# Kernel tuning notes

Measured on AMD Instinct MI355X. Metric: run time of the kernel, lower is better.

## Reference

```python
import jax, jax.numpy as jnp
import numpy as np

EPS = 1e-5  # BatchNorm1d default eps


def _proj_bn(x, W, gamma, beta, mean, var):
    # Conv1d(kernel=1, bias=False) == channel matmul, then inference BatchNorm1d.
    y = jnp.einsum('oc,bcn->bon', W, x)  # (B, C_out, N)
    scale = gamma / jnp.sqrt(var + EPS)  # (C_out,)
    shift = beta - mean * scale
    return y * scale[:, None] + shift[:, None]


def setup_inputs() -> dict:
    key = jax.random.key(0)
    ks = jax.random.split(key, 8)
    B, C, N = 8, 512, 2048
    inp = {
        'input': jax.random.normal(ks[0], (B, C, N), dtype=jnp.float32),
        'Wq': jax.random.normal(ks[1], (C, C), dtype=jnp.float32) * (1.0 / np.sqrt(C)),
        'gq': jnp.ones((C,), jnp.float32),
        'bq': jnp.zeros((C,), jnp.float32),
        'mq': jax.random.normal(ks[2], (C,), dtype=jnp.float32) * 0.1,
        'vq': jax.random.uniform(ks[3], (C,), dtype=jnp.float32) + 0.5,
        'Wk': jax.random.normal(ks[4], (C, C), dtype=jnp.float32) * (1.0 / np.sqrt(C)),
        'gk': jnp.ones((C,), jnp.float32),
        'bk': jnp.zeros((C,), jnp.float32),
        'mk': jax.random.normal(ks[5], (C,), dtype=jnp.float32) * 0.1,
        'vk': jax.random.uniform(ks[6], (C,), dtype=jnp.float32) + 0.5,
        'Wv': jax.random.normal(ks[7], (C, C), dtype=jnp.float32) * (1.0 / np.sqrt(C)),
        'gv': jnp.ones((C,), jnp.float32),
        'bv': jnp.zeros((C,), jnp.float32),
        'mv': jax.random.normal(jax.random.fold_in(key, 100), (C,), dtype=jnp.float32) * 0.1,
        'vv': jax.random.uniform(jax.random.fold_in(key, 101), (C,), dtype=jnp.float32) + 0.5,
    }
    return inp


def reference(input, Wq, gq, bq, mq, vq, Wk, gk, bk, mk, vk, Wv, gv, bv, mv, vv):
    q = _proj_bn(input, Wq, gq, bq, mq, vq)  # (B, C, N)
    k = _proj_bn(input, Wk, gk, bk, mk, vk)
    v = _proj_bn(input, Wv, gv, bv, mv, vv)
    # w[b, i, j] = sum_c q[b, c, i] * k[b, c, j]
    w = jnp.einsum('bci,bcj->bij', q, k)
    a = jax.nn.softmax(w, axis=-1)  # softmax over key axis j (dim 3 in torch)
    # c[b, c, i] = sum_j a[b, i, j] * v[b, c, j]  (== (v * w.softmax(3)).sum(3))
    return jnp.einsum('bij,bcj->bci', a, v)
```

## Files before the change

kernel.cpp:

```cpp
#include <hip/hip_runtime.h>
#include <cstdint>
#include <cstddef>

#define EPSV 1e-5f
constexpr int B_ = 8;
constexpr int C_ = 512;
constexpr int N_ = 2048;

typedef _Float16 f16x8 __attribute__((ext_vector_type(8)));
typedef float    f32x4 __attribute__((ext_vector_type(4)));

__device__ __forceinline__ unsigned short f16b(float f) {
    _Float16 h = (_Float16)f;
    return __builtin_bit_cast(unsigned short, h);
}

__device__ __forceinline__ void gload_lds16(const void* g, void* l) {
    __builtin_amdgcn_global_load_lds(
        (const __attribute__((address_space(1))) void*)g,
        (__attribute__((address_space(3))) void*)l, 16, 0, 0);
}

__global__ __launch_bounds__(256) void split_x_kernel(
    const float* __restrict__ x, unsigned short* __restrict__ xh)
{
    __shared__ float T[64][65];
    const int b = blockIdx.z, c0 = blockIdx.y * 64, n0 = blockIdx.x * 64;
    const float* xb = x + ((size_t)b * C_ + c0) * N_ + n0;
    const int tid = threadIdx.x;
    const int lr = tid >> 4;
    const int lcn = (tid & 15) * 4;
#pragma unroll
    for (int it = 0; it < 4; ++it) {
        float4 v = *(const float4*)&xb[(size_t)(lr + 16 * it) * N_ + lcn];
        T[lr + 16 * it][lcn + 0] = v.x;
        T[lr + 16 * it][lcn + 1] = v.y;
        T[lr + 16 * it][lcn + 2] = v.z;
        T[lr + 16 * it][lcn + 3] = v.w;
    }
    __syncthreads();
    const int n = tid >> 2, cb = (tid & 3) * 16;
    alignas(16) unsigned short h[16];
#pragma unroll
    for (int i = 0; i < 16; ++i)
        h[i] = f16b(T[cb + i][n]);
    const size_t o = ((size_t)b * N_ + n0 + n) * C_ + c0 + cb;
    *(uint4*)&xh[o]     = *(uint4*)&h[0];
    *(uint4*)&xh[o + 8] = *(uint4*)&h[8];
}

__global__ __launch_bounds__(256) void split_w_kernel(
    const float* __restrict__ W, unsigned short* __restrict__ wh)
{
    const int i = (blockIdx.x * 256 + threadIdx.x) * 4;
    float4 v = *(const float4*)&W[i];
    alignas(8) unsigned short h[4];
    h[0] = f16b(v.x); h[1] = f16b(v.y); h[2] = f16b(v.z); h[3] = f16b(v.w);
    *(ushort4*)&wh[i] = *(ushort4*)&h[0];
}

__global__ __launch_bounds__(512) void param_concat_kernel(
    const float* gq, const float* bq, const float* mq, const float* vq,
    const float* gk, const float* bk, const float* mk, const float* vk,
    const float* gv, const float* bv, const float* mv, const float* vv,
    float* sg, float* sb, float* sm, float* sv)
{
    const int i = threadIdx.x;
    sg[i] = gq[i];  sg[512 + i] = gk[i];  sg[1024 + i] = gv[i];
    sb[i] = bq[i];  sb[512 + i] = bk[i];  sb[1024 + i] = bv[i];
    sm[i] = mq[i];  sm[512 + i] = mk[i];  sm[1024 + i] = mv[i];
    sv[i] = vq[i];  sv[512 + i] = vk[i];  sv[1024 + i] = vv[i];
}

constexpr int EPI_QK = 0, EPI_PROJT = 2;

template <int EPI>
__global__ __launch_bounds__(512, 4) void qk256(
    const unsigned short* __restrict__ Ah, const unsigned short* __restrict__ Bh,
    int K, int lda, int ldb,
    long strideA, long strideB, long strideC, long strideC2,
    void* __restrict__ C0, void* __restrict__ C1, float* __restrict__ ML,
    const float* __restrict__ g, const float* __restrict__ bt,
    const float* __restrict__ mu, const float* __restrict__ var)
{
    __shared__ char smem[49152];

    const int id = blockIdx.x;
    const int bz = id & 7;
    const int s  = id >> 3;
    const int bx = s & 15, by = s >> 4;
    const int n0 = bx * 128;
    const int m0 = by * 256;

    const unsigned short* Ahb = Ah + (size_t)bz * strideA;
    const unsigned short* Bhb = Bh + (size_t)bz * strideB;

    const int tid  = threadIdx.x;
    const int lane = tid & 63;
    const int wv   = tid >> 6;
    const int wr   = wv >> 1, wc = wv & 1;
    const int WRB  = wr * 64, WCB = wc * 64;
    const int l4 = lane >> 4, l15 = lane & 15;

#define STAGE(t)                                                              \
    {                                                                         \
        char* dst = smem + ((t) & 1) * 24576;                                 \
        _Pragma("unroll")                                                     \
        for (int u = 0; u < 2; ++u) {                                         \
            const int L = u * 512 + tid;                                      \
            const int row = L >> 2;                                           \
            const int ssl = ((L & 3) ^ ((row >> 1) & 3)) * 8;                 \
            gload_lds16(Ahb + (size_t)(m0 + row) * lda + (t) * 32 + ssl,      \
                        dst + L * 16);                                        \
        }                                                                     \
        {                                                                     \
            const int row = tid >> 2;                                         \
            const int ssl = ((tid & 3) ^ ((row >> 1) & 3)) * 8;               \
            gload_lds16(Bhb + (size_t)(n0 + row) * ldb + (t) * 32 + ssl,      \
                        dst + 16384 + tid * 16);                              \
        }                                                                     \
    }

    f32x4 acc[4][4] = {};
    const int NT = K / 32;

    STAGE(0);

    for (int t = 0; t < NT; ++t) {
        char* cur = smem + (t & 1) * 24576;
        __builtin_amdgcn_s_barrier();
        if (t + 1 < NT) {
            STAGE(t + 1);
            asm volatile("s_waitcnt vmcnt(3)" ::: "memory");
        } else {
            asm volatile("s_waitcnt vmcnt(0)" ::: "memory");
        }
        __builtin_amdgcn_s_barrier();

        f16x8 ah[4], bh[4];
#pragma unroll
        for (int m = 0; m < 4; ++m) {
            const int row = WRB + m * 16 + l15;
            ah[m] = *(const f16x8*)(cur + row * 64 +
                                    ((l4 ^ ((row >> 1) & 3)) * 16));
        }
#pragma unroll
        for (int n = 0; n < 4; ++n) {
            const int row = WCB + n * 16 + l15;
            bh[n] = *(const f16x8*)(cur + 16384 + row * 64 +
                                    ((l4 ^ ((row >> 1) & 3)) * 16));
        }
        __builtin_amdgcn_s_setprio(1);
#pragma unroll
        for (int m = 0; m < 4; ++m)
#pragma unroll
            for (int n = 0; n < 4; ++n)
                acc[m][n] = __builtin_amdgcn_mfma_f32_16x16x32_f16(
                    ah[m], bh[n], acc[m][n], 0, 0, 0);
        __builtin_amdgcn_s_setprio(0);
    }
#undef STAGE

    if constexpr (EPI == EPI_QK) {
        unsigned short* H = (unsigned short*)C0 + (size_t)bz * strideC;
        const int tcol = bx * 2 + wc;
        const size_t mbase = (((size_t)bz * 32 + tcol) * 2) * 2048;
#pragma unroll
        for (int m = 0; m < 4; ++m) {
#pragma unroll
            for (int r = 0; r < 4; ++r) {
                float mx = fmaxf(fmaxf(acc[m][0][r], acc[m][1][r]),
                                 fmaxf(acc[m][2][r], acc[m][3][r]));
#pragma unroll
                for (int off = 1; off < 16; off <<= 1)
                    mx = fmaxf(mx, __shfl_xor(mx, off));
                float pe[4];
                float s2 = 0.f;
#pragma unroll
                for (int n = 0; n < 4; ++n) {
                    pe[n] = __expf(acc[m][n][r] - mx);
                    s2 += pe[n];
                }
#pragma unroll
                for (int off = 1; off < 16; off <<= 1)
                    s2 += __shfl_xor(s2, off);
                const int rloc = WRB + m * 16 + l4 * 4 + r;
                if (l15 == 0) {
                    ML[mbase + m0 + rloc] = mx;
                    ML[mbase + 2048 + m0 + rloc] = s2;
                }
#pragma unroll
                for (int n = 0; n < 4; ++n)
                    H[(size_t)(m0 + rloc) * 2048 + n0 + WCB + n * 16 + l15] =
                        f16b(pe[n]);
            }
        }
    } else {
        if (m0 < 1024) {
            unsigned short* H = (unsigned short*)C0 + (size_t)bz * strideC;
#pragma unroll
            for (int m = 0; m < 4; ++m) {
                const int mg = m0 + WRB + m * 16 + l4 * 4;
                float sc[4], sh[4];
#pragma unroll
                for (int r = 0; r < 4; ++r) {
                    const int o = mg + r;
                    sc[r] = g[o] * rsqrtf(var[o] + EPSV);
                    sh[r] = bt[o] - mu[o] * sc[r];
                }
#pragma unroll
                for (int n = 0; n < 4; ++n) {
                    const int ng = n0 + WCB + n * 16 + l15;
                    alignas(8) unsigned short h4[4];
#pragma unroll
                    for (int r = 0; r < 4; ++r)
                        h4[r] = f16b(acc[m][n][r] * sc[r] + sh[r]);
                    *(ushort4*)&H[(size_t)ng * 1024 + mg] = *(ushort4*)&h4[0];
                }
            }
        } else {
            unsigned short* V = (unsigned short*)C1 + (size_t)bz * strideC2;
#pragma unroll
            for (int m = 0; m < 4; ++m) {
                const int mg = m0 + WRB + m * 16 + l4 * 4;
                float sc[4], sh[4];
#pragma unroll
                for (int r = 0; r < 4; ++r) {
                    const int o = mg + r;
                    sc[r] = g[o] * rsqrtf(var[o] + EPSV);
                    sh[r] = bt[o] - mu[o] * sc[r];
                }
                const int d0 = mg - 1024;
#pragma unroll
                for (int n = 0; n < 4; ++n) {
                    const int ng = n0 + WCB + n * 16 + l15;
#pragma unroll
                    for (int r = 0; r < 4; ++r)
                        V[(size_t)(d0 + r) * 2048 + ng] =
                            f16b(acc[m][n][r] * sc[r] + sh[r]);
                }
            }
        }
    }
}

__global__ __launch_bounds__(512, 2) void pv256(
    const unsigned short* __restrict__ Ah, const unsigned short* __restrict__ Bh,
    int K, int lda, int ldb, long strideA, long strideB, long strideC,
    void* __restrict__ C0,
    const float* __restrict__ corr, const float* __restrict__ linv)
{
    constexpr int BUFSZ = 49152;
    __shared__ char smem[163840];

    const int id = blockIdx.x;
    const int bz = id & 7;
    const int s  = id >> 3;
    const int bx = s & 3, by = s >> 2;
    const int n0 = bx * 128;
    const int m0 = by * 256;

    const unsigned short* Ahb = Ah + (size_t)bz * strideA;
    const unsigned short* Bhb = Bh + (size_t)bz * strideB;

    const int tid  = threadIdx.x;
    const int lane = tid & 63;
    const int wv   = tid >> 6;
    const int wr   = wv >> 2, wc = wv & 3;
    const int WRB  = wr * 128, WCB = wc * 32;
    const int l4 = lane >> 4, l15 = lane & 15;

    const int srow = tid >> 3;
    const int sslot = ((tid & 7) ^ (srow & 7)) * 8;

    unsigned short* corrLds = (unsigned short*)(smem + 147456);
    for (int idx = tid; idx < 2048; idx += 512) {
        const int t = idx >> 6, i4 = (idx & 63) * 4;
        float4 c4 = *(const float4*)&corr[((size_t)bz * 32 + t) * 2048 + m0 + i4];
        alignas(8) unsigned short h4[4] =
            {f16b(c4.x), f16b(c4.y), f16b(c4.z), f16b(c4.w)};
        *(ushort4*)&corrLds[(size_t)t * 256 + i4] = *(ushort4*)&h4[0];
    }
    __syncthreads();

#define STAGE(t)                                                              \
    {                                                                         \
        char* dst = smem + ((t) % 3) * BUFSZ;                                 \
        const unsigned short* asrc =                                          \
            Ahb + (size_t)(m0 + srow) * lda + (t) * 64 + sslot;               \
        _Pragma("unroll")                                                     \
        for (int u = 0; u < 4; ++u)                                           \
            gload_lds16(asrc + (size_t)(u * 64) * lda,                        \
                        dst + u * 8192 + tid * 16);                           \
        const unsigned short* bsrc =                                          \
            Bhb + (size_t)(n0 + srow) * ldb + (t) * 64 + sslot;               \
        _Pragma("unroll")                                                     \
        for (int u = 0; u < 2; ++u)                                           \
            gload_lds16(bsrc + (size_t)(u * 64) * ldb,                        \
                        dst + 32768 + u * 8192 + tid * 16);                   \
    }

    f32x4 acc[8][2] = {};
    const int NT = K / 64;

    STAGE(0);
    STAGE(1);

    for (int t = 0; t < NT; ++t) {
        char* cur = smem + (t % 3) * BUFSZ;
        if (t + 2 < NT) {
            asm volatile("s_waitcnt vmcnt(6)" ::: "memory");
        } else {
            asm volatile("s_waitcnt vmcnt(0)" ::: "memory");
        }
        __builtin_amdgcn_s_barrier();
        asm volatile("" ::: "memory");
        if (t + 2 < NT) STAGE(t + 2);

        f16x8 ah[8][2], bh[2][2];
#pragma unroll
        for (int m = 0; m < 8; ++m) {
            const int row = WRB + m * 16 + l15;
#pragma unroll
            for (int kk = 0; kk < 2; ++kk)
                ah[m][kk] = *(const f16x8*)(cur + row * 128 +
                                            (((kk << 2) | l4) ^ (row & 7)) * 16);
        }
#pragma unroll
        for (int n = 0; n < 2; ++n) {
            const int row = WCB + n * 16 + l15;
#pragma unroll
            for (int kk = 0; kk < 2; ++kk)
                bh[n][kk] = *(const f16x8*)(cur + 32768 + row * 128 +
                                            (((kk << 2) | l4) ^ (row & 7)) * 16);
        }
#pragma unroll
        for (int m = 0; m < 8; ++m) {
            const _Float16 cf = ((const _Float16*)corrLds)
                [(size_t)t * 256 + WRB + m * 16 + l15];
            ah[m][0] = ah[m][0] * cf;
            ah[m][1] = ah[m][1] * cf;
        }
        __builtin_amdgcn_s_setprio(1);
#pragma unroll
        for (int kk = 0; kk < 2; ++kk)
#pragma unroll
            for (int m = 0; m < 8; ++m)
#pragma unroll
                for (int n = 0; n < 2; ++n)
                    acc[m][n] = __builtin_amdgcn_mfma_f32_16x16x32_f16(
                        ah[m][kk], bh[n][kk], acc[m][n], 0, 0, 0);
        __builtin_amdgcn_s_setprio(0);
    }
#undef STAGE

    float* Cb = (float*)C0 + (size_t)bz * strideC;
    const float* lb = linv + (size_t)bz * 2048;
#pragma unroll
    for (int m = 0; m < 8; ++m) {
        const int mrow = m0 + WRB + m * 16 + l4 * 4;
        float lv[4];
#pragma unroll
        for (int r = 0; r < 4; ++r)
            lv[r] = lb[mrow + r];
#pragma unroll
        for (int n = 0; n < 2; ++n) {
            const int col = n0 + WCB + n * 16 + l15;
            float4 o4 = make_float4(acc[m][n][0] * lv[0],
                                    acc[m][n][1] * lv[1],
                                    acc[m][n][2] * lv[2],
                                    acc[m][n][3] * lv[3]);
            *(float4*)&Cb[(size_t)col * 2048 + mrow] = o4;
        }
    }
}

__global__ __launch_bounds__(256) void ml_combine_kernel(
    const float* __restrict__ ml, float* __restrict__ corr,
    float* __restrict__ linv)
{
    const int idx = blockIdx.x * 256 + threadIdx.x;
    const int b = idx >> 11, i = idx & 2047;
    const float* base = ml + ((size_t)b * 32) * 2 * 2048 + i;
    float M = -3.0e38f;
#pragma unroll 8
    for (int t = 0; t < 32; ++t)
        M = fmaxf(M, base[(size_t)t * 4096]);
    float L = 0.f;
    float* cb = corr + (size_t)b * 32 * 2048 + i;
#pragma unroll 8
    for (int t = 0; t < 32; ++t) {
        const float c = __expf(base[(size_t)t * 4096] - M);
        L += c * base[(size_t)t * 4096 + 2048];
        cb[(size_t)t * 2048] = c;
    }
    linv[idx] = 1.0f / L;
}

extern "C" void kernel_launch(void* const* d_in, const int* in_sizes, int n_in,
                              void* d_out, int out_size, void* d_ws, size_t ws_size,
                              hipStream_t stream)
{
    (void)in_sizes; (void)n_in; (void)out_size; (void)ws_size;
    const float* x  = (const float*)d_in[0];
    const float* Wq = (const float*)d_in[1];
    const float* gq = (const float*)d_in[2];
    const float* bq = (const float*)d_in[3];
    const float* mq = (const float*)d_in[4];
    const float* vq = (const float*)d_in[5];
    const float* Wk = (const float*)d_in[6];
    const float* gk = (const float*)d_in[7];
    const float* bk = (const float*)d_in[8];
    const float* mk = (const float*)d_in[9];
    const float* vk = (const float*)d_in[10];
    const float* Wv = (const float*)d_in[11];
    const float* gv = (const float*)d_in[12];
    const float* bv = (const float*)d_in[13];
    const float* mv = (const float*)d_in[14];
    const float* vv = (const float*)d_in[15];
    float* out = (float*)d_out;

    const size_t MiB = 1048576;
    char* ws = (char*)d_ws;
    unsigned short* Wst = (unsigned short*)(ws);
    unsigned short* Wqh = Wst;
    unsigned short* Wkh = Wst + 512 * 512;
    unsigned short* Wvh = Wst + 1024 * 512;
    unsigned short* vbf  = (unsigned short*)(ws + 2 * MiB);
    unsigned short* qkTh = (unsigned short*)(ws + 18 * MiB);
    unsigned short* xTh  = (unsigned short*)(ws + 50 * MiB);
    unsigned short* pbuf = (unsigned short*)(ws + 66 * MiB);
    float* mlbuf = (float*)(ws + 130 * MiB);
    float* corr  = (float*)(ws + 134 * MiB);
    float* linv  = (float*)(ws + 136 * MiB);
    float* sg = (float*)(ws + 136 * MiB + 65536);
    float* sb = sg + 1536;
    float* sm = sb + 1536;
    float* sv = sm + 1536;

    const long BS = (long)N_ * C_;
    const long QKS = (long)N_ * 1024;

    split_x_kernel<<<dim3(N_ / 64, C_ / 64, B_), 256, 0, stream>>>(x, xTh);
    split_w_kernel<<<dim3(256), 256, 0, stream>>>(Wq, Wqh);
    split_w_kernel<<<dim3(256), 256, 0, stream>>>(Wk, Wkh);
    split_w_kernel<<<dim3(256), 256, 0, stream>>>(Wv, Wvh);
    param_concat_kernel<<<dim3(1), 512, 0, stream>>>(
        gq, bq, mq, vq, gk, bk, mk, vk, gv, bv, mv, vv, sg, sb, sm, sv);

    qk256<EPI_PROJT><<<dim3(768), 512, 0, stream>>>(
        Wst, xTh, 512, 512, 512, 0, BS, QKS, BS, qkTh, vbf,
        nullptr, sg, sb, sm, sv);

    qk256<EPI_QK><<<dim3(1024), 512, 0, stream>>>(
        qkTh, qkTh + 512, 512, 1024, 1024, QKS, QKS, (long)N_ * N_, 0,
        pbuf, nullptr, mlbuf, nullptr, nullptr, nullptr, nullptr);

    ml_combine_kernel<<<dim3(B_ * N_ / 256), 256, 0, stream>>>(
        mlbuf, corr, linv);

    pv256<<<dim3(256), 512, 0, stream>>>(
        pbuf, vbf, 2048, 2048, 2048, (long)N_ * N_, BS, BS, out, corr, linv);
}
```

Before: 169.4 us.

## Shrink PV tile to 128x128 with double buffering and fuse weight prep kernels

Replaces the 256x128, 512-thread, triple-buffered PV GEMM with a 128x128, 256-thread, double-buffered version launched on 512 blocks. Each wave now holds a 4x4 accumulator tile. The smaller shared-memory footprint should allow more blocks per CU and fill the GPU with more blocks. The three weight-conversion launches and the parameter concat launch are merged into one kernel to cut launch overhead. In exchange, each block reuses loaded data less, and prefetch depth drops from two stages ahead to one.

```diff
diff --git a/kernel.cpp b/kernel.cpp
--- a/kernel.cpp
+++ b/kernel.cpp
@@ -49,27 +49,34 @@
     *(uint4*)&xh[o + 8] = *(uint4*)&h[8];
 }
 
-__global__ __launch_bounds__(256) void split_w_kernel(
-    const float* __restrict__ W, unsigned short* __restrict__ wh)
-{
-    const int i = (blockIdx.x * 256 + threadIdx.x) * 4;
-    float4 v = *(const float4*)&W[i];
-    alignas(8) unsigned short h[4];
-    h[0] = f16b(v.x); h[1] = f16b(v.y); h[2] = f16b(v.z); h[3] = f16b(v.w);
-    *(ushort4*)&wh[i] = *(ushort4*)&h[0];
-}
-
-__global__ __launch_bounds__(512) void param_concat_kernel(
+__global__ __launch_bounds__(256) void split_w_all_kernel(
+    const float* __restrict__ Wq, const float* __restrict__ Wk,
+    const float* __restrict__ Wv, unsigned short* __restrict__ wst,
     const float* gq, const float* bq, const float* mq, const float* vq,
     const float* gk, const float* bk, const float* mk, const float* vk,
     const float* gv, const float* bv, const float* mv, const float* vv,
     float* sg, float* sb, float* sm, float* sv)
 {
-    const int i = threadIdx.x;
-    sg[i] = gq[i];  sg[512 + i] = gk[i];  sg[1024 + i] = gv[i];
-    sb[i] = bq[i];  sb[512 + i] = bk[i];  sb[1024 + i] = bv[i];
-    sm[i] = mq[i];  sm[512 + i] = mk[i];  sm[1024 + i] = mv[i];
-    sv[i] = vq[i];  sv[512 + i] = vk[i];  sv[1024 + i] = vv[i];
+    const int blk = blockIdx.x;
+    if (blk < 768) {
+        const int i = blk * 1024 + threadIdx.x * 4;
+        const int which = i >> 18;
+        const int off = i & 262143;
+        const float* W = (which == 0) ? Wq : (which == 1) ? Wk : Wv;
+        float4 v = *(const float4*)&W[off];
+        alignas(8) unsigned short h[4];
+        h[0] = f16b(v.x); h[1] = f16b(v.y); h[2] = f16b(v.z); h[3] = f16b(v.w);
+        *(ushort4*)&wst[i] = *(ushort4*)&h[0];
+    } else {
+#pragma unroll
+        for (int u = 0; u < 2; ++u) {
+            const int i = threadIdx.x + u * 256;
+            sg[i] = gq[i];  sg[512 + i] = gk[i];  sg[1024 + i] = gv[i];
+            sb[i] = bq[i];  sb[512 + i] = bk[i];  sb[1024 + i] = bv[i];
+            sm[i] = mq[i];  sm[512 + i] = mk[i];  sm[1024 + i] = mv[i];
+            sv[i] = vq[i];  sv[512 + i] = vk[i];  sv[1024 + i] = vv[i];
+        }
+    }
 }
 
 constexpr int EPI_QK = 0, EPI_PROJT = 2;
@@ -244,21 +251,20 @@
     }
 }
 
-__global__ __launch_bounds__(512, 2) void pv256(
+__global__ __launch_bounds__(256, 2) void pv128(
     const unsigned short* __restrict__ Ah, const unsigned short* __restrict__ Bh,
     int K, int lda, int ldb, long strideA, long strideB, long strideC,
     void* __restrict__ C0,
     const float* __restrict__ corr, const float* __restrict__ linv)
 {
-    constexpr int BUFSZ = 49152;
-    __shared__ char smem[163840];
+    __shared__ char smem[73728];
 
     const int id = blockIdx.x;
     const int bz = id & 7;
     const int s  = id >> 3;
     const int bx = s & 3, by = s >> 2;
     const int n0 = bx * 128;
-    const int m0 = by * 256;
+    const int m0 = by * 128;
 
     const unsigned short* Ahb = Ah + (size_t)bz * strideA;
     const unsigned short* Bhb = Bh + (size_t)bz * strideB;
@@ -266,60 +272,63 @@
     const int tid  = threadIdx.x;
     const int lane = tid & 63;
     const int wv   = tid >> 6;
-    const int wr   = wv >> 2, wc = wv & 3;
-    const int WRB  = wr * 128, WCB = wc * 32;
+    const int wr   = wv >> 1, wc = wv & 1;
+    const int WRB  = wr * 64, WCB = wc * 64;
     const int l4 = lane >> 4, l15 = lane & 15;
 
-    const int srow = tid >> 3;
-    const int sslot = ((tid & 7) ^ (srow & 7)) * 8;
-
-    unsigned short* corrLds = (unsigned short*)(smem + 147456);
-    for (int idx = tid; idx < 2048; idx += 512) {
-        const int t = idx >> 6, i4 = (idx & 63) * 4;
+    const int NT = K / 64;
+
+    unsigned short* corrLds = (unsigned short*)(smem + 65536);
+#pragma unroll
+    for (int u = 0; u < 4; ++u) {
+        const int idx = u * 256 + tid;
+        const int t = idx >> 5, i4 = (idx & 31) * 4;
         float4 c4 = *(const float4*)&corr[((size_t)bz * 32 + t) * 2048 + m0 + i4];
         alignas(8) unsigned short h4[4] =
             {f16b(c4.x), f16b(c4.y), f16b(c4.z), f16b(c4.w)};
-        *(ushort4*)&corrLds[(size_t)t * 256 + i4] = *(ushort4*)&h4[0];
+        *(ushort4*)&corrLds[(size_t)t * 128 + i4] = *(ushort4*)&h4[0];
     }
     __syncthreads();
 
 #define STAGE(t)                                                              \
     {                                                                         \
-        char* dst = smem + ((t) % 3) * BUFSZ;                                 \
-        const unsigned short* asrc =                                          \
-            Ahb + (size_t)(m0 + srow) * lda + (t) * 64 + sslot;               \
+        char* dst = smem + ((t) & 1) * 32768;                                 \
         _Pragma("unroll")                                                     \
-        for (int u = 0; u < 4; ++u)                                           \
-            gload_lds16(asrc + (size_t)(u * 64) * lda,                        \
-                        dst + u * 8192 + tid * 16);                           \
-        const unsigned short* bsrc =                                          \
-            Bhb + (size_t)(n0 + srow) * ldb + (t) * 64 + sslot;               \
+        for (int u = 0; u < 4; ++u) {                                         \
+            const int L = u * 256 + tid;                                      \
+            const int row = L >> 3;                                           \
+            const int ssl = ((L & 7) ^ (row & 7)) * 8;                        \
+            gload_lds16(Ahb + (size_t)(m0 + row) * lda + (t) * 64 + ssl,      \
+                        dst + L * 16);                                        \
+        }                                                                     \
         _Pragma("unroll")                                                     \
-        for (int u = 0; u < 2; ++u)                                           \
-            gload_lds16(bsrc + (size_t)(u * 64) * ldb,                        \
-                        dst + 32768 + u * 8192 + tid * 16);                   \
-    }
-
-    f32x4 acc[8][2] = {};
-    const int NT = K / 64;
+        for (int u = 0; u < 4; ++u) {                                         \
+            const int L = u * 256 + tid;                                      \
+            const int row = L >> 3;                                           \
+            const int ssl = ((L & 7) ^ (row & 7)) * 8;                        \
+            gload_lds16(Bhb + (size_t)(n0 + row) * ldb + (t) * 64 + ssl,      \
+                        dst + 16384 + L * 16);                                \
+        }                                                                     \
+    }
+
+    f32x4 acc[4][4] = {};
 
     STAGE(0);
-    STAGE(1);
 
     for (int t = 0; t < NT; ++t) {
-        char* cur = smem + (t % 3) * BUFSZ;
-        if (t + 2 < NT) {
-            asm volatile("s_waitcnt vmcnt(6)" ::: "memory");
+        char* cur = smem + (t & 1) * 32768;
+        __builtin_amdgcn_s_barrier();
+        if (t + 1 < NT) {
+            STAGE(t + 1);
+            asm volatile("s_waitcnt vmcnt(8)" ::: "memory");
         } else {
             asm volatile("s_waitcnt vmcnt(0)" ::: "memory");
         }
         __builtin_amdgcn_s_barrier();
-        asm volatile("" ::: "memory");
-        if (t + 2 < NT) STAGE(t + 2);
-
-        f16x8 ah[8][2], bh[2][2];
-#pragma unroll
-        for (int m = 0; m < 8; ++m) {
+
+        f16x8 ah[4][2], bh[4][2];
+#pragma unroll
+        for (int m = 0; m < 4; ++m) {
             const int row = WRB + m * 16 + l15;
 #pragma unroll
             for (int kk = 0; kk < 2; ++kk)
@@ -327,17 +336,17 @@
                                             (((kk << 2) | l4) ^ (row & 7)) * 16);
         }
 #pragma unroll
-        for (int n = 0; n < 2; ++n) {
+        for (int n = 0; n < 4; ++n) {
             const int row = WCB + n * 16 + l15;
 #pragma unroll
             for (int kk = 0; kk < 2; ++kk)
-                bh[n][kk] = *(const f16x8*)(cur + 32768 + row * 128 +
+                bh[n][kk] = *(const f16x8*)(cur + 16384 + row * 128 +
                                             (((kk << 2) | l4) ^ (row & 7)) * 16);
         }
 #pragma unroll
-        for (int m = 0; m < 8; ++m) {
+        for (int m = 0; m < 4; ++m) {
             const _Float16 cf = ((const _Float16*)corrLds)
-                [(size_t)t * 256 + WRB + m * 16 + l15];
+                [(size_t)t * 128 + WRB + m * 16 + l15];
             ah[m][0] = ah[m][0] * cf;
             ah[m][1] = ah[m][1] * cf;
         }
@@ -345,9 +354,9 @@
 #pragma unroll
         for (int kk = 0; kk < 2; ++kk)
 #pragma unroll
-            for (int m = 0; m < 8; ++m)
-#pragma unroll
-                for (int n = 0; n < 2; ++n)
+            for (int m = 0; m < 4; ++m)
+#pragma unroll
+                for (int n = 0; n < 4; ++n)
                     acc[m][n] = __builtin_amdgcn_mfma_f32_16x16x32_f16(
                         ah[m][kk], bh[n][kk], acc[m][n], 0, 0, 0);
         __builtin_amdgcn_s_setprio(0);
@@ -357,14 +366,14 @@
     float* Cb = (float*)C0 + (size_t)bz * strideC;
     const float* lb = linv + (size_t)bz * 2048;
 #pragma unroll
-    for (int m = 0; m < 8; ++m) {
+    for (int m = 0; m < 4; ++m) {
         const int mrow = m0 + WRB + m * 16 + l4 * 4;
         float lv[4];
 #pragma unroll
         for (int r = 0; r < 4; ++r)
             lv[r] = lb[mrow + r];
 #pragma unroll
-        for (int n = 0; n < 2; ++n) {
+        for (int n = 0; n < 4; ++n) {
             const int col = n0 + WCB + n * 16 + l15;
             float4 o4 = make_float4(acc[m][n][0] * lv[0],
                                     acc[m][n][1] * lv[1],
@@ -423,9 +432,6 @@
     const size_t MiB = 1048576;
     char* ws = (char*)d_ws;
     unsigned short* Wst = (unsigned short*)(ws);
-    unsigned short* Wqh = Wst;
-    unsigned short* Wkh = Wst + 512 * 512;
-    unsigned short* Wvh = Wst + 1024 * 512;
     unsigned short* vbf  = (unsigned short*)(ws + 2 * MiB);
     unsigned short* qkTh = (unsigned short*)(ws + 18 * MiB);
     unsigned short* xTh  = (unsigned short*)(ws + 50 * MiB);
@@ -442,10 +448,8 @@
     const long QKS = (long)N_ * 1024;
 
     split_x_kernel<<<dim3(N_ / 64, C_ / 64, B_), 256, 0, stream>>>(x, xTh);
-    split_w_kernel<<<dim3(256), 256, 0, stream>>>(Wq, Wqh);
-    split_w_kernel<<<dim3(256), 256, 0, stream>>>(Wk, Wkh);
-    split_w_kernel<<<dim3(256), 256, 0, stream>>>(Wv, Wvh);
-    param_concat_kernel<<<dim3(1), 512, 0, stream>>>(
+    split_w_all_kernel<<<dim3(769), 256, 0, stream>>>(
+        Wq, Wk, Wv, Wst,
         gq, bq, mq, vq, gk, bk, mk, vk, gv, bv, mv, vv, sg, sb, sm, sv);
 
     qk256<EPI_PROJT><<<dim3(768), 512, 0, stream>>>(
@@ -459,6 +463,6 @@
     ml_combine_kernel<<<dim3(B_ * N_ / 256), 256, 0, stream>>>(
         mlbuf, corr, linv);
 
-    pv256<<<dim3(256), 512, 0, stream>>>(
+    pv128<<<dim3(512), 256, 0, stream>>>(
         pbuf, vbf, 2048, 2048, 2048, (long)N_ * N_, BS, BS, out, corr, linv);
 }
```

Measured after the change: 158.0 us. 6.7% less time.
